# Kernel optimization log

Measured on AMD Instinct MI355X. Metric: run time of the kernel, lower is better.

The kernel has to match this reference:

```python
import jax, jax.numpy as jnp
import numpy as np


def prelu(x, a):
    return jnp.where(x >= 0, x, a * x)


def setup_inputs() -> dict:
    key = jax.random.key(0)
    ks = jax.random.split(key, 16)
    B, N, S, D = 4, 400, 512, 100
    rn = lambda k, shape, s=1.0: jax.random.normal(k, shape, dtype=jnp.float32) * s
    W = 0.05  # weight scale to keep activations sane
    return {
        "x": rn(ks[0], (B, N, D)),
        "G": rn(ks[1], (1, S, N), W),
        "A": rn(ks[2], (1, S, N), W),
        "W_gf": rn(ks[3], (D, N), W), "b_gf": rn(ks[4], (D,), W),
        "a_gf": jnp.float32(0.25),
        "Wg": rn(ks[5], (D, S), W), "bg": rn(ks[6], (D,), W),
        "W4a": rn(ks[7], (D, 2 * D), W), "b4a": rn(ks[8], (D,), W),
        "a4a": jnp.float32(0.25),
        "W4b": rn(ks[9], (1, D), W), "b4b": rn(ks[10], (1,), W),
        "a4b": jnp.float32(0.25),
        "W5": rn(ks[11], (D, D), W), "b5": rn(ks[12], (D,), W),
        "a5": jnp.float32(0.25),
    }


def reference(x, G, A, W_gf, b_gf, a_gf, Wg, bg, W4a, b4a, a4a, W4b, b4b, a4b, W5, b5, a5):
    B, N, D = x.shape          # (4, 400, 100)
    S = A.shape[1]             # 512
    # G1 = PReLU(Linear(G))  -> (1, S, D)
    G1 = prelu(jnp.einsum('osn,dn->osd', G, W_gf) + b_gf, a_gf)
    # A @ x -> (b, S, D)
    Ax = jnp.einsum('osn,bnd->bsd', A, x)
    # G_AX = G1 @ (A x)^T -> (b, S, S)
    G_AX = jnp.einsum('sd,btd->bst', G1[0], Ax)
    P = jax.nn.softmax(G_AX, axis=-1)                       # (b, S, S)
    # sim(): per-batch euclidean pdist on detached P
    Pd = jax.lax.stop_gradient(P)
    sq = jnp.sum(Pd * Pd, axis=-1)                          # (b, S)
    d2 = sq[:, :, None] + sq[:, None, :] - 2.0 * jnp.einsum('bij,bkj->bik', Pd, Pd)
    eye = jnp.eye(S, dtype=x.dtype)
    dist = jnp.sqrt(jnp.maximum(d2, 0.0)) * (1.0 - eye)     # squareform: zero diag
    # norm(): B = dist + I; D^-1/2 B D^-1/2; then extra .mm(B) (as in source)
    Bm = dist + eye
    dh = jnp.sum(Bm, axis=-1) ** -0.5                       # rowsum >= 1
    M = dh[:, :, None] * Bm * dh[:, None, :]
    adj = jnp.einsum('bij,bjk->bik', M, Bm)                 # (b, S, S)
    # gcn1: relu(Linear(adj @ P)), 512 -> 100
    gx = jax.nn.relu(jnp.einsum('bij,bjd->bid', adj, P) @ Wg.T + bg)  # (b, S, D)
    # tiled concat + MLP: Linear(200,100) split into x-part and gx-part
    h1 = x @ W4a[:, :D].T                                   # (b, N, D)
    h2 = gx @ W4a[:, D:].T                                  # (b, S, D)
    h = prelu(h1[:, :, None, :] + h2[:, None, :, :] + b4a, a4a)  # (b, N, S, D)
    logits = prelu(h @ W4b.T + b4b, a4b)                    # (b, N, S, 1)
    div = jax.nn.softmax(logits, axis=1)[..., 0]            # softmax over N -> (b, N, S)
    out = prelu(jnp.einsum('bns,bsd->bnd', div, gx) @ W5.T + b5, a5) + x
    return out
```

## Files before the change

kernel.cpp:

```cpp
#include <hip/hip_runtime.h>
#include <hip/hip_bf16.h>

#define BB 4
#define NN 400
#define DD 100
#define SS 512

typedef __attribute__((ext_vector_type(8))) short bf16x8;
typedef __attribute__((ext_vector_type(4))) float f32x4;

__device__ __forceinline__ float prelu_f(float v, float a) { return v >= 0.f ? v : a * v; }

__device__ __forceinline__ unsigned short f2bf(float x) {
    union { __hip_bfloat16 h; unsigned short u; } c;
    c.h = __float2bfloat16(x);
    return c.u;
}
__device__ __forceinline__ float bf2f(unsigned short u) {
    return __uint_as_float(((unsigned)u) << 16);
}

__device__ __forceinline__ bf16x8 ldfrag(const unsigned short* rowp, int grp) {
    ushort4 lo = *(const ushort4*)(rowp + grp * 4);
    ushort4 hi = *(const ushort4*)(rowp + grp * 4 + 16);
    bf16x8 r = {(short)lo.x, (short)lo.y, (short)lo.z, (short)lo.w,
                (short)hi.x, (short)hi.y, (short)hi.z, (short)hi.w};
    return r;
}

#define LPAD 136

__global__ __launch_bounds__(256)
void mmfa(const void* __restrict__ Ap, const void* __restrict__ A2p, int lda, int sA,
          const void* __restrict__ Bp, const void* __restrict__ B2p, int ldb, int sB,
          int transB, int flags,
          float* __restrict__ C, int sC, int M, int N, int K,
          int nsplit, int kchunk, int EP,
          const float* __restrict__ bias, const float* __restrict__ alpha,
          const float* __restrict__ rv, int rvStride,
          const float* __restrict__ res, int sRes)
{
    int zz = blockIdx.z;
    int b = zz / nsplit, split = zz - b * nsplit;
    int kbeg = split * kchunk, kend = min(K, kbeg + kchunk);
    int i0 = blockIdx.x * 64, n0 = blockIdx.y * 64;
    if (EP == 5 && i0 > n0) return;

    int tid = threadIdx.x;
    int lane = tid & 63, wave = tid >> 6;
    int r16 = lane & 15, grp = (lane >> 4) & 3;
    int wr = wave >> 1, wc = wave & 1;

    __shared__ unsigned short sa[64][LPAD];
    __shared__ unsigned short sb[64][LPAD];

    f32x4 acc[2][2];
#pragma unroll
    for (int fm = 0; fm < 2; ++fm)
#pragma unroll
        for (int fn = 0; fn < 2; ++fn)
            acc[fm][fn] = (f32x4){0.f, 0.f, 0.f, 0.f};

    for (int kt = kbeg; kt < kend; kt += 128) {
        if (flags & 1) {
            const unsigned short* Ab = (const unsigned short*)Ap + (size_t)b * sA;
#pragma unroll
            for (int it = 0; it < 8; ++it) {
                int idx = tid + it * 256;
                int row = idx >> 5, kq = (idx & 31) * 4;
                ushort4 u = {0, 0, 0, 0};
                if (i0 + row < M && kt + kq + 4 <= kend)
                    u = *(const ushort4*)&Ab[(size_t)(i0 + row) * lda + kt + kq];
                *(ushort4*)&sa[row][kq] = u;
            }
        } else {
            const float* Ab  = (const float*)Ap + (size_t)b * sA;
            const float* Ab2 = A2p ? (const float*)A2p + (size_t)b * sA : nullptr;
#pragma unroll
            for (int it = 0; it < 8; ++it) {
                int idx = tid + it * 256;
                int row = idx >> 5, kq = (idx & 31) * 4;
                float4 v = make_float4(0.f, 0.f, 0.f, 0.f);
                if (i0 + row < M && kt + kq + 4 <= kend) {
                    v = *(const float4*)&Ab[(size_t)(i0 + row) * lda + kt + kq];
                    if (Ab2) {
                        float4 w = *(const float4*)&Ab2[(size_t)(i0 + row) * lda + kt + kq];
                        v.x += w.x; v.y += w.y; v.z += w.z; v.w += w.w;
                    }
                }
                ushort4 u;
                u.x = f2bf(v.x); u.y = f2bf(v.y); u.z = f2bf(v.z); u.w = f2bf(v.w);
                *(ushort4*)&sa[row][kq] = u;
            }
        }
        if (transB) {
            if (flags & 2) {
                const unsigned short* Bb = (const unsigned short*)Bp + (size_t)b * sB;
#pragma unroll
                for (int it = 0; it < 8; ++it) {
                    int idx = tid + it * 256;
                    int row = idx >> 5, kq = (idx & 31) * 4;
                    ushort4 u = {0, 0, 0, 0};
                    if (n0 + row < N && kt + kq + 4 <= kend)
                        u = *(const ushort4*)&Bb[(size_t)(n0 + row) * ldb + kt + kq];
                    *(ushort4*)&sb[row][kq] = u;
                }
            } else {
                const float* Bb  = (const float*)Bp + (size_t)b * sB;
                const float* Bb2 = B2p ? (const float*)B2p + (size_t)b * sB : nullptr;
#pragma unroll
                for (int it = 0; it < 8; ++it) {
                    int idx = tid + it * 256;
                    int row = idx >> 5, kq = (idx & 31) * 4;
                    float4 v = make_float4(0.f, 0.f, 0.f, 0.f);
                    if (n0 + row < N && kt + kq + 4 <= kend) {
                        v = *(const float4*)&Bb[(size_t)(n0 + row) * ldb + kt + kq];
                        if (Bb2) {
                            float4 w = *(const float4*)&Bb2[(size_t)(n0 + row) * ldb + kt + kq];
                            v.x += w.x; v.y += w.y; v.z += w.z; v.w += w.w;
                        }
                    }
                    ushort4 u;
                    u.x = f2bf(v.x); u.y = f2bf(v.y); u.z = f2bf(v.z); u.w = f2bf(v.w);
                    *(ushort4*)&sb[row][kq] = u;
                }
            }
        } else {
            const float* Bb  = (const float*)Bp + (size_t)b * sB;
            const float* Bb2 = B2p ? (const float*)B2p + (size_t)b * sB : nullptr;
#pragma unroll
            for (int it = 0; it < 8; ++it) {
                int idx = tid + it * 256;
                int kk = idx >> 4;
                int nq = (idx & 15) * 4;
                float4 v = make_float4(0.f, 0.f, 0.f, 0.f);
                if (kt + kk < kend && n0 + nq + 4 <= N) {
                    v = *(const float4*)&Bb[(size_t)(kt + kk) * ldb + n0 + nq];
                    if (Bb2) {
                        float4 w = *(const float4*)&Bb2[(size_t)(kt + kk) * ldb + n0 + nq];
                        v.x += w.x; v.y += w.y; v.z += w.z; v.w += w.w;
                    }
                }
                sb[nq + 0][kk] = f2bf(v.x);
                sb[nq + 1][kk] = f2bf(v.y);
                sb[nq + 2][kk] = f2bf(v.z);
                sb[nq + 3][kk] = f2bf(v.w);
            }
        }
        __syncthreads();

#pragma unroll
        for (int ks = 0; ks < 4; ++ks) {
            bf16x8 a0 = ldfrag(&sa[wr * 32 + r16][ks * 32], grp);
            bf16x8 a1 = ldfrag(&sa[wr * 32 + 16 + r16][ks * 32], grp);
            bf16x8 b0 = ldfrag(&sb[wc * 32 + r16][ks * 32], grp);
            bf16x8 b1 = ldfrag(&sb[wc * 32 + 16 + r16][ks * 32], grp);
            acc[0][0] = __builtin_amdgcn_mfma_f32_16x16x32_bf16(a0, b0, acc[0][0], 0, 0, 0);
            acc[0][1] = __builtin_amdgcn_mfma_f32_16x16x32_bf16(a0, b1, acc[0][1], 0, 0, 0);
            acc[1][0] = __builtin_amdgcn_mfma_f32_16x16x32_bf16(a1, b0, acc[1][0], 0, 0, 0);
            acc[1][1] = __builtin_amdgcn_mfma_f32_16x16x32_bf16(a1, b1, acc[1][1], 0, 0, 0);
        }
        __syncthreads();
    }

    if (nsplit > 1) {
        float* Pp = C + (size_t)(b * nsplit + split) * M * N;
#pragma unroll
        for (int fm = 0; fm < 2; ++fm)
#pragma unroll
            for (int fn = 0; fn < 2; ++fn)
#pragma unroll
                for (int reg = 0; reg < 4; ++reg) {
                    int i = i0 + wr * 32 + fm * 16 + grp * 4 + reg;
                    int n = n0 + wc * 32 + fn * 16 + r16;
                    if (i < M && n < N) Pp[(size_t)i * N + n] = acc[fm][fn][reg];
                }
        return;
    }

    float al = alpha ? *alpha : 0.f;
    const float* rvb = rv ? rv + (size_t)b * rvStride : nullptr;
    float* Cb = C + (size_t)b * sC;
#pragma unroll
    for (int fm = 0; fm < 2; ++fm)
#pragma unroll
        for (int fn = 0; fn < 2; ++fn)
#pragma unroll
            for (int reg = 0; reg < 4; ++reg) {
                int i = i0 + wr * 32 + fm * 16 + grp * 4 + reg;
                int n = n0 + wc * 32 + fn * 16 + r16;
                if (i >= M || n >= N) continue;
                float v = acc[fm][fn][reg];
                if (EP == 4) {
                    v = prelu_f(v + bias[n], al) + res[(size_t)b * sRes + (size_t)i * N + n];
                } else if (EP == 5) {
                    float d2 = rvb[i] + rvb[n] - 2.f * v;
                    v = (i == n) ? 1.f : sqrtf(fmaxf(d2, 0.f));
                }
                Cb[(size_t)i * N + n] = v;
                if (EP == 5) Cb[(size_t)n * N + i] = v;
            }
}

__global__ __launch_bounds__(256)
void k_reduce(const float* __restrict__ part, int nsplit, float* __restrict__ C, int sC,
              int M, int N, int EP, const float* __restrict__ bias,
              const float* __restrict__ alpha, const float* __restrict__ rv, int rvStride)
{
    int b = blockIdx.y;
    int MN = M * N;
    int flat = (blockIdx.x * 256 + threadIdx.x) * 4;
    if (flat >= MN) return;
    const float* p = part + (size_t)b * nsplit * MN + flat;
    float4 v = *(const float4*)p;
    for (int s = 1; s < nsplit; ++s) {
        float4 w = *(const float4*)(p + (size_t)s * MN);
        v.x += w.x; v.y += w.y; v.z += w.z; v.w += w.w;
    }
    float o[4] = {v.x, v.y, v.z, v.w};
    int i = flat / N, n = flat - i * N;
    if (EP == 1) {
        float al = *alpha;
#pragma unroll
        for (int j = 0; j < 4; ++j) o[j] = prelu_f(o[j] + bias[n + j], al);
    } else if (EP == 2) {
        float r = rv[(size_t)b * rvStride + i];
#pragma unroll
        for (int j = 0; j < 4; ++j) o[j] *= r;
    } else if (EP == 3) {
        float r = rv[(size_t)b * rvStride + i];
#pragma unroll
        for (int j = 0; j < 4; ++j) { float t = r * o[j] + bias[n + j]; o[j] = t > 0.f ? t : 0.f; }
    }
    float* co = C + (size_t)b * sC + flat;
    *(float4*)co = make_float4(o[0], o[1], o[2], o[3]);
}

__global__ __launch_bounds__(256)
void kbm(const float* __restrict__ parts, const float* __restrict__ sq,
         float* __restrict__ Bm)
{
    int b = blockIdx.y;
    int flat = (blockIdx.x * 256 + threadIdx.x) * 4;
    int i = flat / SS, n0 = flat - i * SS;
    const float* pb = parts + (size_t)b * 4 * SS * SS;
    const float* sqb = sq + (size_t)b * SS;
    float o[4];
#pragma unroll
    for (int j = 0; j < 4; ++j) {
        int n = n0 + j;
        int lo = min(i, n), hi = max(i, n);
        size_t idx = (size_t)lo * SS + hi;
        float d = pb[idx] + pb[(size_t)SS * SS + idx]
                + pb[2 * (size_t)SS * SS + idx] + pb[3 * (size_t)SS * SS + idx];
        float d2 = sqb[i] + sqb[n] - 2.f * d;
        o[j] = (i == n) ? 1.f : sqrtf(fmaxf(d2, 0.f));
    }
    *(float4*)&Bm[(size_t)b * SS * SS + flat] = make_float4(o[0], o[1], o[2], o[3]);
}

__global__ __launch_bounds__(512)
void k_softmax_sq(const float* __restrict__ scores, unsigned short* __restrict__ Pb,
                  float* __restrict__ sq)
{
    int row = blockIdx.x;
    int t = threadIdx.x;
    int w = t >> 6, lane = t & 63;
    __shared__ float sm[8];

    float v = scores[(size_t)row * SS + t];
    float m = v;
    for (int off = 32; off; off >>= 1) m = fmaxf(m, __shfl_xor(m, off, 64));
    if (lane == 0) sm[w] = m;
    __syncthreads();
    m = sm[0];
#pragma unroll
    for (int i = 1; i < 8; ++i) m = fmaxf(m, sm[i]);
    __syncthreads();

    float e = expf(v - m);
    float s = e;
    for (int off = 32; off; off >>= 1) s += __shfl_xor(s, off, 64);
    if (lane == 0) sm[w] = s;
    __syncthreads();
    s = 0.f;
#pragma unroll
    for (int i = 0; i < 8; ++i) s += sm[i];
    __syncthreads();

    unsigned short u = f2bf(e / s);
    Pb[(size_t)row * SS + t] = u;
    float pf = bf2f(u);
    float q = pf * pf;
    for (int off = 32; off; off >>= 1) q += __shfl_xor(q, off, 64);
    if (lane == 0) sm[w] = q;
    __syncthreads();
    if (t == 0) {
        float r = 0.f;
#pragma unroll
        for (int i = 0; i < 8; ++i) r += sm[i];
        sq[row] = r;
    }
}

__global__ __launch_bounds__(512)
void k_dh(const float* __restrict__ Bm, float* __restrict__ dh)
{
    int row = blockIdx.x;
    int t = threadIdx.x;
    int w = t >> 6, lane = t & 63;
    __shared__ float sm[8];
    float v = Bm[(size_t)row * SS + t];
    for (int off = 32; off; off >>= 1) v += __shfl_xor(v, off, 64);
    if (lane == 0) sm[w] = v;
    __syncthreads();
    if (t == 0) {
        float r = 0.f;
#pragma unroll
        for (int i = 0; i < 8; ++i) r += sm[i];
        dh[row] = rsqrtf(r);
    }
}

__global__ __launch_bounds__(256)
void k_div8(const float* __restrict__ h1, const float* __restrict__ h2,
            const float* __restrict__ b4a, const float* __restrict__ a4ap,
            const float* __restrict__ W4b, const float* __restrict__ b4bp,
            const float* __restrict__ a4bp, float* __restrict__ divT)
{
    int b = blockIdx.y;
    int s0 = blockIdx.x * 8;
    int tid = threadIdx.x;

    __shared__ float sh[8][104];
    __shared__ float sw[100];
    __shared__ float L[8][400];

    for (int idx = tid; idx < 800; idx += 256) {
        int s = idx / 100, d = idx - 100 * s;
        sh[s][d] = h2[((size_t)(b * SS + s0 + s)) * DD + d] + b4a[d];
    }
    if (tid < 100) sw[tid] = W4b[tid];
    __syncthreads();

    float a4a = *a4ap, a4b = *a4bp, b4b = *b4bp;

    for (int n = tid; n < NN; n += 256) {
        const float* h1r = &h1[((size_t)b * NN + n) * DD];
        float accs[8] = {0.f, 0.f, 0.f, 0.f, 0.f, 0.f, 0.f, 0.f};
        for (int j = 0; j < DD; j += 4) {
            float4 hv = *(const float4*)&h1r[j];
            float4 wv = *(const float4*)&sw[j];
#pragma unroll
            for (int s = 0; s < 8; ++s) {
                float4 cv = *(const float4*)&sh[s][j];
                float x0 = hv.x + cv.x; x0 = x0 > 0.f ? x0 : a4a * x0;
                float x1 = hv.y + cv.y; x1 = x1 > 0.f ? x1 : a4a * x1;
                float x2 = hv.z + cv.z; x2 = x2 > 0.f ? x2 : a4a * x2;
                float x3 = hv.w + cv.w; x3 = x3 > 0.f ? x3 : a4a * x3;
                accs[s] += x0 * wv.x + x1 * wv.y + x2 * wv.z + x3 * wv.w;
            }
        }
#pragma unroll
        for (int s = 0; s < 8; ++s) L[s][n] = prelu_f(accs[s] + b4b, a4b);
    }
    __syncthreads();

    int w = tid >> 6, lane = tid & 63;
    for (int si = w; si < 8; si += 4) {
        float m = -INFINITY;
        for (int n = lane; n < NN; n += 64) m = fmaxf(m, L[si][n]);
        for (int off = 32; off; off >>= 1) m = fmaxf(m, __shfl_xor(m, off, 64));
        float ss = 0.f;
        for (int n = lane; n < NN; n += 64) {
            float e = expf(L[si][n] - m);
            L[si][n] = e;
            ss += e;
        }
        for (int off = 32; off; off >>= 1) ss += __shfl_xor(ss, off, 64);
        float inv = 1.f / ss;
        for (int n = lane; n < NN; n += 64)
            divT[((size_t)b * NN + n) * SS + s0 + si] = L[si][n] * inv;
    }
}

extern "C" void kernel_launch(void* const* d_in, const int* in_sizes, int n_in,
                              void* d_out, int out_size, void* d_ws, size_t ws_size,
                              hipStream_t stream) {
    const float* x   = (const float*)d_in[0];
    const float* G   = (const float*)d_in[1];
    const float* Am  = (const float*)d_in[2];
    const float* Wgf = (const float*)d_in[3];
    const float* bgf = (const float*)d_in[4];
    const float* agf = (const float*)d_in[5];
    const float* Wg  = (const float*)d_in[6];
    const float* bg  = (const float*)d_in[7];
    const float* W4a = (const float*)d_in[8];
    const float* b4a = (const float*)d_in[9];
    const float* a4a = (const float*)d_in[10];
    const float* W4b = (const float*)d_in[11];
    const float* b4b = (const float*)d_in[12];
    const float* a4b = (const float*)d_in[13];
    const float* W5  = (const float*)d_in[14];
    const float* b5  = (const float*)d_in[15];
    const float* a5  = (const float*)d_in[16];
    float* out = (float*)d_out;

    float* ws = (float*)d_ws;
    float* G1   = ws + 0;
    float* G1P  = ws + 51200;
    float* AXP  = ws + 256000;
    float* SC   = ws + 665600;
    float* BM   = ws + 1714176;
    float* SQ   = ws + 2762752;
    float* DH   = ws + 2764800;
    float* PDP  = ws + 2766848;
    float* PWP  = ws + 6961152;
    float* PW   = ws + 7780352;
    float* T1P  = ws + 7985152;
    float* T1   = ws + 8804352;
    float* GXP  = ws + 9009152;
    float* GX   = ws + 9828352;
    float* H1   = ws + 10033152;
    float* H2   = ws + 10193152;
    float* DV   = ws + 10397952;
    float* TMPP = ws + 11217152;
    float* TMP  = ws + 11857152;
    unsigned short* PB = (unsigned short*)(ws + 12017152);

    mmfa<<<dim3(8, 2, 4), 256, 0, stream>>>(G, nullptr, NN, 0, Wgf, nullptr, NN, 0, 1, 0,
        G1P, 0, SS, DD, NN, 4, 100, 0, nullptr, nullptr, nullptr, 0, nullptr, 0);
    k_reduce<<<dim3(50, 1), 256, 0, stream>>>(G1P, 4, G1, SS * DD, SS, DD, 1, bgf, agf, nullptr, 0);
    mmfa<<<dim3(8, 2, 2 * BB), 256, 0, stream>>>(Am, nullptr, NN, 0, x, nullptr, DD, NN * DD, 0, 0,
        AXP, 0, SS, DD, NN, 2, 200, 0, nullptr, nullptr, nullptr, 0, nullptr, 0);
    mmfa<<<dim3(8, 8, BB), 256, 0, stream>>>(G1, nullptr, DD, 0,
        AXP, AXP + SS * DD, DD, 2 * SS * DD, 1, 0,
        SC, SS * SS, SS, SS, DD, 1, DD, 0, nullptr, nullptr, nullptr, 0, nullptr, 0);
    k_softmax_sq<<<BB * SS, 512, 0, stream>>>(SC, PB, SQ);
    mmfa<<<dim3(8, 8, 4 * BB), 256, 0, stream>>>(PB, nullptr, SS, SS * SS, PB, nullptr, SS, SS * SS, 1, 3,
        PDP, 0, SS, SS, SS, 4, 128, 5, nullptr, nullptr, nullptr, 0, nullptr, 0);
    kbm<<<dim3(256, BB), 256, 0, stream>>>(PDP, SQ, BM);
    k_dh<<<BB * SS, 512, 0, stream>>>(BM, DH);
    mmfa<<<dim3(8, 2, 4 * BB), 256, 0, stream>>>(PB, nullptr, SS, SS * SS, Wg, nullptr, SS, 0, 1, 1,
        PWP, 0, SS, DD, SS, 4, 128, 0, nullptr, nullptr, nullptr, 0, nullptr, 0);
    k_reduce<<<dim3(50, BB), 256, 0, stream>>>(PWP, 4, PW, SS * DD, SS, DD, 0, nullptr, nullptr, nullptr, 0);
    mmfa<<<dim3(8, 2, 4 * BB), 256, 0, stream>>>(BM, nullptr, SS, SS * SS, PW, nullptr, DD, SS * DD, 0, 0,
        T1P, 0, SS, DD, SS, 4, 128, 0, nullptr, nullptr, nullptr, 0, nullptr, 0);
    k_reduce<<<dim3(50, BB), 256, 0, stream>>>(T1P, 4, T1, SS * DD, SS, DD, 2, nullptr, nullptr, DH, SS);
    mmfa<<<dim3(8, 2, 4 * BB), 256, 0, stream>>>(BM, nullptr, SS, SS * SS, T1, nullptr, DD, SS * DD, 0, 0,
        GXP, 0, SS, DD, SS, 4, 128, 0, nullptr, nullptr, nullptr, 0, nullptr, 0);
    k_reduce<<<dim3(50, BB), 256, 0, stream>>>(GXP, 4, GX, SS * DD, SS, DD, 3, bg, nullptr, DH, SS);
    mmfa<<<dim3(7, 2, BB), 256, 0, stream>>>(x, nullptr, DD, NN * DD, W4a, nullptr, 2 * DD, 0, 1, 0,
        H1, NN * DD, NN, DD, DD, 1, DD, 0, nullptr, nullptr, nullptr, 0, nullptr, 0);
    mmfa<<<dim3(8, 2, BB), 256, 0, stream>>>(GX, nullptr, DD, SS * DD, W4a + DD, nullptr, 2 * DD, 0, 1, 0,
        H2, SS * DD, SS, DD, DD, 1, DD, 0, nullptr, nullptr, nullptr, 0, nullptr, 0);
    k_div8<<<dim3(SS / 8, BB), 256, 0, stream>>>(H1, H2, b4a, a4a, W4b, b4b, a4b, DV);
    mmfa<<<dim3(7, 2, 4 * BB), 256, 0, stream>>>(DV, nullptr, SS, NN * SS, GX, nullptr, DD, SS * DD, 0, 0,
        TMPP, 0, NN, DD, SS, 4, 128, 0, nullptr, nullptr, nullptr, 0, nullptr, 0);
    k_reduce<<<dim3(40, BB), 256, 0, stream>>>(TMPP, 4, TMP, NN * DD, NN, DD, 0, nullptr, nullptr, nullptr, 0);
    mmfa<<<dim3(7, 2, BB), 256, 0, stream>>>(TMP, nullptr, DD, NN * DD, W5, nullptr, DD, 0, 1, 0,
        out, NN * DD, NN, DD, DD, 1, DD, 4, b5, a5, nullptr, 0, x, NN * DD);
}
```

Measured before the change: 276.5 us.

## Merge independent GEMMs into combined launches and fold reductions into consumer loads

Factors the GEMM body into a device function so that independent GEMMs (G·Wgf, A·x, x·W4a, and the Gram matrix with P·Wg) can share a single launch, with work selected by block index. Split-K partials are now summed inside the next GEMM's operand load instead of in separate reduce kernels. The D^-1/2 scaling is applied as a per-row B-operand scale and in the epilogue. The row-sum and rsqrt step is folded into the Bm construction kernel. Together these cut the number of kernel launches and intermediate round trips through memory, at the cost of lower split-K parallelism in some GEMMs and more per-load arithmetic.

```diff
diff --git a/kernel.cpp b/kernel.cpp
--- a/kernel.cpp
+++ b/kernel.cpp
@@ -5,6 +5,8 @@
 #define NN 400
 #define DD 100
 #define SS 512
+#define LPAD 136
+#define SMEM_BYTES (64 * LPAD * 2 * 2)
 
 typedef __attribute__((ext_vector_type(8))) short bf16x8;
 typedef __attribute__((ext_vector_type(4))) float f32x4;
@@ -28,32 +30,22 @@
     return r;
 }
 
-#define LPAD 136
-
-__global__ __launch_bounds__(256)
-void mmfa(const void* __restrict__ Ap, const void* __restrict__ A2p, int lda, int sA,
-          const void* __restrict__ Bp, const void* __restrict__ B2p, int ldb, int sB,
-          int transB, int flags,
-          float* __restrict__ C, int sC, int M, int N, int K,
-          int nsplit, int kchunk, int EP,
-          const float* __restrict__ bias, const float* __restrict__ alpha,
-          const float* __restrict__ rv, int rvStride,
-          const float* __restrict__ res, int sRes)
-{
-    int zz = blockIdx.z;
-    int b = zz / nsplit, split = zz - b * nsplit;
-    int kbeg = split * kchunk, kend = min(K, kbeg + kchunk);
-    int i0 = blockIdx.x * 64, n0 = blockIdx.y * 64;
-    if (EP == 5 && i0 > n0) return;
-
+__device__ __forceinline__ void mm_dev(char* smemraw,
+    const void* Ap, const void* A2p, int aBf, int lda,
+    const void* Bp, const void* B2p, int bBf, int ldb, int transB,
+    const float* bscale,
+    int i0, int n0, int M, int N, int kbeg, int kend,
+    float* C, int ldc, int EP,
+    const float* bias, const float* alphaP, const float* rv,
+    const float* res, int resLd)
+{
+    unsigned short (*sa)[LPAD] = (unsigned short(*)[LPAD])smemraw;
+    unsigned short (*sb)[LPAD] = (unsigned short(*)[LPAD])(smemraw + 64 * LPAD * 2);
     int tid = threadIdx.x;
     int lane = tid & 63, wave = tid >> 6;
     int r16 = lane & 15, grp = (lane >> 4) & 3;
     int wr = wave >> 1, wc = wave & 1;
 
-    __shared__ unsigned short sa[64][LPAD];
-    __shared__ unsigned short sb[64][LPAD];
-
     f32x4 acc[2][2];
 #pragma unroll
     for (int fm = 0; fm < 2; ++fm)
@@ -62,8 +54,8 @@
             acc[fm][fn] = (f32x4){0.f, 0.f, 0.f, 0.f};
 
     for (int kt = kbeg; kt < kend; kt += 128) {
-        if (flags & 1) {
-            const unsigned short* Ab = (const unsigned short*)Ap + (size_t)b * sA;
+        if (aBf) {
+            const unsigned short* Ab = (const unsigned short*)Ap;
 #pragma unroll
             for (int it = 0; it < 8; ++it) {
                 int idx = tid + it * 256;
@@ -74,8 +66,8 @@
                 *(ushort4*)&sa[row][kq] = u;
             }
         } else {
-            const float* Ab  = (const float*)Ap + (size_t)b * sA;
-            const float* Ab2 = A2p ? (const float*)A2p + (size_t)b * sA : nullptr;
+            const float* Ab  = (const float*)Ap;
+            const float* Ab2 = (const float*)A2p;
 #pragma unroll
             for (int it = 0; it < 8; ++it) {
                 int idx = tid + it * 256;
@@ -94,8 +86,8 @@
             }
         }
         if (transB) {
-            if (flags & 2) {
-                const unsigned short* Bb = (const unsigned short*)Bp + (size_t)b * sB;
+            if (bBf) {
+                const unsigned short* Bb = (const unsigned short*)Bp;
 #pragma unroll
                 for (int it = 0; it < 8; ++it) {
                     int idx = tid + it * 256;
@@ -106,8 +98,8 @@
                     *(ushort4*)&sb[row][kq] = u;
                 }
             } else {
-                const float* Bb  = (const float*)Bp + (size_t)b * sB;
-                const float* Bb2 = B2p ? (const float*)B2p + (size_t)b * sB : nullptr;
+                const float* Bb  = (const float*)Bp;
+                const float* Bb2 = (const float*)B2p;
 #pragma unroll
                 for (int it = 0; it < 8; ++it) {
                     int idx = tid + it * 256;
@@ -126,8 +118,8 @@
                 }
             }
         } else {
-            const float* Bb  = (const float*)Bp + (size_t)b * sB;
-            const float* Bb2 = B2p ? (const float*)B2p + (size_t)b * sB : nullptr;
+            const float* Bb  = (const float*)Bp;
+            const float* Bb2 = (const float*)B2p;
 #pragma unroll
             for (int it = 0; it < 8; ++it) {
                 int idx = tid + it * 256;
@@ -140,6 +132,10 @@
                         float4 w = *(const float4*)&Bb2[(size_t)(kt + kk) * ldb + n0 + nq];
                         v.x += w.x; v.y += w.y; v.z += w.z; v.w += w.w;
                     }
+                    if (bscale) {
+                        float s = bscale[kt + kk];
+                        v.x *= s; v.y *= s; v.z *= s; v.w *= s;
+                    }
                 }
                 sb[nq + 0][kk] = f2bf(v.x);
                 sb[nq + 1][kk] = f2bf(v.y);
@@ -163,24 +159,7 @@
         __syncthreads();
     }
 
-    if (nsplit > 1) {
-        float* Pp = C + (size_t)(b * nsplit + split) * M * N;
-#pragma unroll
-        for (int fm = 0; fm < 2; ++fm)
-#pragma unroll
-            for (int fn = 0; fn < 2; ++fn)
-#pragma unroll
-                for (int reg = 0; reg < 4; ++reg) {
-                    int i = i0 + wr * 32 + fm * 16 + grp * 4 + reg;
-                    int n = n0 + wc * 32 + fn * 16 + r16;
-                    if (i < M && n < N) Pp[(size_t)i * N + n] = acc[fm][fn][reg];
-                }
-        return;
-    }
-
-    float al = alpha ? *alpha : 0.f;
-    const float* rvb = rv ? rv + (size_t)b * rvStride : nullptr;
-    float* Cb = C + (size_t)b * sC;
+    float al = alphaP ? *alphaP : 0.f;
 #pragma unroll
     for (int fm = 0; fm < 2; ++fm)
 #pragma unroll
@@ -191,15 +170,147 @@
                 int n = n0 + wc * 32 + fn * 16 + r16;
                 if (i >= M || n >= N) continue;
                 float v = acc[fm][fn][reg];
-                if (EP == 4) {
-                    v = prelu_f(v + bias[n], al) + res[(size_t)b * sRes + (size_t)i * N + n];
-                } else if (EP == 5) {
-                    float d2 = rvb[i] + rvb[n] - 2.f * v;
+                if (EP == 1) v = prelu_f(v + bias[n], al);
+                else if (EP == 2) v *= rv[i];
+                else if (EP == 3) { float t = rv[i] * v + bias[n]; v = t > 0.f ? t : 0.f; }
+                else if (EP == 4) v = prelu_f(v + bias[n], al) + res[(size_t)i * resLd + n];
+                else if (EP == 5) {
+                    float d2 = rv[i] + rv[n] - 2.f * v;
                     v = (i == n) ? 1.f : sqrtf(fmaxf(d2, 0.f));
                 }
-                Cb[(size_t)i * N + n] = v;
-                if (EP == 5) Cb[(size_t)n * N + i] = v;
+                C[(size_t)i * ldc + n] = v;
+                if (EP == 5) C[(size_t)n * ldc + i] = v;
             }
+}
+
+__global__ __launch_bounds__(256)
+void mmfa(const void* Ap, const void* A2p, int lda, int sA,
+          const void* Bp, const void* B2p, int ldb, int sB,
+          int transB, int flags,
+          const float* bscale, int bscaleStride,
+          float* C, int sC, int M, int N, int K,
+          int nsplit, int kchunk, int EP,
+          const float* bias, const float* alpha,
+          const float* rv, int rvStride,
+          const float* res, int sRes)
+{
+    __shared__ __align__(16) char sm[SMEM_BYTES];
+    int zz = blockIdx.z;
+    int b = zz / nsplit, split = zz - b * nsplit;
+    int kbeg = split * kchunk, kend = min(K, kbeg + kchunk);
+    int i0 = blockIdx.x * 64, n0 = blockIdx.y * 64;
+    if (EP == 5 && i0 > n0) return;
+
+    const void* Ab; const void* Ab2 = nullptr;
+    if (flags & 1) Ab = (const void*)((const unsigned short*)Ap + (size_t)b * sA);
+    else {
+        Ab = (const void*)((const float*)Ap + (size_t)b * sA);
+        if (A2p) Ab2 = (const void*)((const float*)A2p + (size_t)b * sA);
+    }
+    const void* Bb; const void* Bb2 = nullptr;
+    if (flags & 2) Bb = (const void*)((const unsigned short*)Bp + (size_t)b * sB);
+    else {
+        Bb = (const void*)((const float*)Bp + (size_t)b * sB);
+        if (B2p) Bb2 = (const void*)((const float*)B2p + (size_t)b * sB);
+    }
+    const float* bs = bscale ? bscale + (size_t)b * bscaleStride : nullptr;
+
+    float* Cd; int ep;
+    if (nsplit > 1) { Cd = C + (size_t)(b * nsplit + split) * M * N; ep = 0; }
+    else            { Cd = C + (size_t)b * sC; ep = EP; }
+    const float* rvb = rv ? rv + (size_t)b * rvStride : nullptr;
+    const float* resb = res ? res + (size_t)b * sRes : nullptr;
+
+    mm_dev(sm, Ab, Ab2, flags & 1, lda, Bb, Bb2, flags & 2, ldb, transB, bs,
+           i0, n0, M, N, kbeg, kend, Cd, N, ep, bias, alpha, rvb, resb, N);
+}
+
+__global__ __launch_bounds__(256)
+void preU(const float* G, const float* Wgf, const float* Am, const float* x,
+          const float* W4a, float* G1P, float* AXP, float* H1)
+{
+    __shared__ __align__(16) char sm[SMEM_BYTES];
+    int t = blockIdx.x;
+    if (t < 64) {
+        int split = t >> 4, rem = t & 15, ix = rem >> 1, iy = rem & 1;
+        mm_dev(sm, G, nullptr, 0, NN, Wgf, nullptr, 0, NN, 1, nullptr,
+               ix * 64, iy * 64, SS, DD, split * 100, split * 100 + 100,
+               G1P + (size_t)split * SS * DD, DD, 0,
+               nullptr, nullptr, nullptr, nullptr, 0);
+    } else if (t < 192) {
+        int u = t - 64;
+        int b = u >> 5, rem = u & 31, split = rem >> 4, r2 = rem & 15;
+        int ix = r2 >> 1, iy = r2 & 1;
+        mm_dev(sm, Am, nullptr, 0, NN, x + (size_t)b * NN * DD, nullptr, 0, DD, 0, nullptr,
+               ix * 64, iy * 64, SS, DD, split * 200, split * 200 + 200,
+               AXP + (size_t)(b * 2 + split) * SS * DD, DD, 0,
+               nullptr, nullptr, nullptr, nullptr, 0);
+    } else {
+        int u = t - 192;
+        int b = u / 14, rem = u % 14, ix = rem >> 1, iy = rem & 1;
+        mm_dev(sm, x + (size_t)b * NN * DD, nullptr, 0, DD, W4a, nullptr, 0, 2 * DD, 1, nullptr,
+               ix * 64, iy * 64, NN, DD, 0, DD,
+               H1 + (size_t)b * NN * DD, DD, 0,
+               nullptr, nullptr, nullptr, nullptr, 0);
+    }
+}
+
+__global__ __launch_bounds__(256)
+void gramU(const unsigned short* PB, const float* Wg, float* PDP, float* PWP)
+{
+    __shared__ __align__(16) char sm[SMEM_BYTES];
+    int t = blockIdx.x;
+    if (t < 1024) {
+        int z = t >> 6, rem = t & 63, ix = rem >> 3, iy = rem & 7;
+        if (ix > iy) return;
+        int b = z >> 2, split = z & 3;
+        const unsigned short* Pbb = PB + (size_t)b * SS * SS;
+        mm_dev(sm, Pbb, nullptr, 1, SS, Pbb, nullptr, 1, SS, 1, nullptr,
+               ix * 64, iy * 64, SS, SS, split * 128, split * 128 + 128,
+               PDP + (size_t)(b * 4 + split) * SS * SS, SS, 0,
+               nullptr, nullptr, nullptr, nullptr, 0);
+    } else {
+        int u = t - 1024;
+        int z = u >> 4, rem = u & 15, ix = rem >> 1, iy = rem & 1;
+        int b = z >> 1, split = z & 1;
+        mm_dev(sm, PB + (size_t)b * SS * SS, nullptr, 1, SS, Wg, nullptr, 0, SS, 1, nullptr,
+               ix * 64, iy * 64, SS, DD, split * 256, split * 256 + 256,
+               PWP + (size_t)(b * 2 + split) * SS * DD, DD, 0,
+               nullptr, nullptr, nullptr, nullptr, 0);
+    }
+}
+
+__global__ __launch_bounds__(256)
+void kbm2(const float* __restrict__ parts, const float* __restrict__ sq,
+          float* __restrict__ Bm, float* __restrict__ dh)
+{
+    __shared__ float red[4];
+    int b = blockIdx.y;
+    int tid = threadIdx.x;
+    int flat = (blockIdx.x * 256 + tid) * 4;
+    int i = flat / SS, n0 = flat - i * SS;
+    const float* pb = parts + (size_t)b * 4 * SS * SS;
+    const float* sqb = sq + (size_t)b * SS;
+    float o[4];
+#pragma unroll
+    for (int j = 0; j < 4; ++j) {
+        int n = n0 + j;
+        int lo = min(i, n), hi = max(i, n);
+        size_t idx = (size_t)lo * SS + hi;
+        float d = pb[idx] + pb[(size_t)SS * SS + idx]
+                + pb[2 * (size_t)SS * SS + idx] + pb[3 * (size_t)SS * SS + idx];
+        float d2 = sqb[i] + sqb[n] - 2.f * d;
+        o[j] = (i == n) ? 1.f : sqrtf(fmaxf(d2, 0.f));
+    }
+    *(float4*)&Bm[(size_t)b * SS * SS + flat] = make_float4(o[0], o[1], o[2], o[3]);
+
+    float rs = o[0] + o[1] + o[2] + o[3];
+    for (int off = 32; off; off >>= 1) rs += __shfl_xor(rs, off, 64);
+    int lane = tid & 63, wave = tid >> 6;
+    if (lane == 0) red[wave] = rs;
+    __syncthreads();
+    if (tid == 0)   dh[(size_t)b * SS + blockIdx.x * 2]     = rsqrtf(red[0] + red[1]);
+    if (tid == 128) dh[(size_t)b * SS + blockIdx.x * 2 + 1] = rsqrtf(red[2] + red[3]);
 }
 
 __global__ __launch_bounds__(256)
@@ -236,29 +347,6 @@
     *(float4*)co = make_float4(o[0], o[1], o[2], o[3]);
 }
 
-__global__ __launch_bounds__(256)
-void kbm(const float* __restrict__ parts, const float* __restrict__ sq,
-         float* __restrict__ Bm)
-{
-    int b = blockIdx.y;
-    int flat = (blockIdx.x * 256 + threadIdx.x) * 4;
-    int i = flat / SS, n0 = flat - i * SS;
-    const float* pb = parts + (size_t)b * 4 * SS * SS;
-    const float* sqb = sq + (size_t)b * SS;
-    float o[4];
-#pragma unroll
-    for (int j = 0; j < 4; ++j) {
-        int n = n0 + j;
-        int lo = min(i, n), hi = max(i, n);
-        size_t idx = (size_t)lo * SS + hi;
-        float d = pb[idx] + pb[(size_t)SS * SS + idx]
-                + pb[2 * (size_t)SS * SS + idx] + pb[3 * (size_t)SS * SS + idx];
-        float d2 = sqb[i] + sqb[n] - 2.f * d;
-        o[j] = (i == n) ? 1.f : sqrtf(fmaxf(d2, 0.f));
-    }
-    *(float4*)&Bm[(size_t)b * SS * SS + flat] = make_float4(o[0], o[1], o[2], o[3]);
-}
-
 __global__ __launch_bounds__(512)
 void k_softmax_sq(const float* __restrict__ scores, unsigned short* __restrict__ Pb,
                   float* __restrict__ sq)
@@ -300,25 +388,6 @@
 #pragma unroll
         for (int i = 0; i < 8; ++i) r += sm[i];
         sq[row] = r;
-    }
-}
-
-__global__ __launch_bounds__(512)
-void k_dh(const float* __restrict__ Bm, float* __restrict__ dh)
-{
-    int row = blockIdx.x;
-    int t = threadIdx.x;
-    int w = t >> 6, lane = t & 63;
-    __shared__ float sm[8];
-    float v = Bm[(size_t)row * SS + t];
-    for (int off = 32; off; off >>= 1) v += __shfl_xor(v, off, 64);
-    if (lane == 0) sm[w] = v;
-    __syncthreads();
-    if (t == 0) {
-        float r = 0.f;
-#pragma unroll
-        for (int i = 0; i < 8; ++i) r += sm[i];
-        dh[row] = rsqrtf(r);
     }
 }
 
@@ -416,48 +485,36 @@
     float* DH   = ws + 2764800;
     float* PDP  = ws + 2766848;
     float* PWP  = ws + 6961152;
-    float* PW   = ws + 7780352;
-    float* T1P  = ws + 7985152;
-    float* T1   = ws + 8804352;
-    float* GXP  = ws + 9009152;
-    float* GX   = ws + 9828352;
-    float* H1   = ws + 10033152;
-    float* H2   = ws + 10193152;
-    float* DV   = ws + 10397952;
-    float* TMPP = ws + 11217152;
-    float* TMP  = ws + 11857152;
-    unsigned short* PB = (unsigned short*)(ws + 12017152);
-
-    mmfa<<<dim3(8, 2, 4), 256, 0, stream>>>(G, nullptr, NN, 0, Wgf, nullptr, NN, 0, 1, 0,
-        G1P, 0, SS, DD, NN, 4, 100, 0, nullptr, nullptr, nullptr, 0, nullptr, 0);
+    float* T1P  = ws + 7370752;
+    float* GX   = ws + 7780352;
+    float* H1   = ws + 7985152;
+    float* H2   = ws + 8145152;
+    float* DV   = ws + 8349952;
+    float* TMPP = ws + 9169152;
+    unsigned short* PB = (unsigned short*)(ws + 9489152);
+
+    preU<<<248, 256, 0, stream>>>(G, Wgf, Am, x, W4a, G1P, AXP, H1);
     k_reduce<<<dim3(50, 1), 256, 0, stream>>>(G1P, 4, G1, SS * DD, SS, DD, 1, bgf, agf, nullptr, 0);
-    mmfa<<<dim3(8, 2, 2 * BB), 256, 0, stream>>>(Am, nullptr, NN, 0, x, nullptr, DD, NN * DD, 0, 0,
-        AXP, 0, SS, DD, NN, 2, 200, 0, nullptr, nullptr, nullptr, 0, nullptr, 0);
     mmfa<<<dim3(8, 8, BB), 256, 0, stream>>>(G1, nullptr, DD, 0,
-        AXP, AXP + SS * DD, DD, 2 * SS * DD, 1, 0,
+        AXP, AXP + SS * DD, DD, 2 * SS * DD, 1, 0, nullptr, 0,
         SC, SS * SS, SS, SS, DD, 1, DD, 0, nullptr, nullptr, nullptr, 0, nullptr, 0);
     k_softmax_sq<<<BB * SS, 512, 0, stream>>>(SC, PB, SQ);
-    mmfa<<<dim3(8, 8, 4 * BB), 256, 0, stream>>>(PB, nullptr, SS, SS * SS, PB, nullptr, SS, SS * SS, 1, 3,
-        PDP, 0, SS, SS, SS, 4, 128, 5, nullptr, nullptr, nullptr, 0, nullptr, 0);
-    kbm<<<dim3(256, BB), 256, 0, stream>>>(PDP, SQ, BM);
-    k_dh<<<BB * SS, 512, 0, stream>>>(BM, DH);
-    mmfa<<<dim3(8, 2, 4 * BB), 256, 0, stream>>>(PB, nullptr, SS, SS * SS, Wg, nullptr, SS, 0, 1, 1,
-        PWP, 0, SS, DD, SS, 4, 128, 0, nullptr, nullptr, nullptr, 0, nullptr, 0);
-    k_reduce<<<dim3(50, BB), 256, 0, stream>>>(PWP, 4, PW, SS * DD, SS, DD, 0, nullptr, nullptr, nullptr, 0);
-    mmfa<<<dim3(8, 2, 4 * BB), 256, 0, stream>>>(BM, nullptr, SS, SS * SS, PW, nullptr, DD, SS * DD, 0, 0,
-        T1P, 0, SS, DD, SS, 4, 128, 0, nullptr, nullptr, nullptr, 0, nullptr, 0);
-    k_reduce<<<dim3(50, BB), 256, 0, stream>>>(T1P, 4, T1, SS * DD, SS, DD, 2, nullptr, nullptr, DH, SS);
-    mmfa<<<dim3(8, 2, 4 * BB), 256, 0, stream>>>(BM, nullptr, SS, SS * SS, T1, nullptr, DD, SS * DD, 0, 0,
-        GXP, 0, SS, DD, SS, 4, 128, 0, nullptr, nullptr, nullptr, 0, nullptr, 0);
-    k_reduce<<<dim3(50, BB), 256, 0, stream>>>(GXP, 4, GX, SS * DD, SS, DD, 3, bg, nullptr, DH, SS);
-    mmfa<<<dim3(7, 2, BB), 256, 0, stream>>>(x, nullptr, DD, NN * DD, W4a, nullptr, 2 * DD, 0, 1, 0,
-        H1, NN * DD, NN, DD, DD, 1, DD, 0, nullptr, nullptr, nullptr, 0, nullptr, 0);
-    mmfa<<<dim3(8, 2, BB), 256, 0, stream>>>(GX, nullptr, DD, SS * DD, W4a + DD, nullptr, 2 * DD, 0, 1, 0,
+    gramU<<<1152, 256, 0, stream>>>(PB, Wg, PDP, PWP);
+    kbm2<<<dim3(256, BB), 256, 0, stream>>>(PDP, SQ, BM, DH);
+    mmfa<<<dim3(8, 2, 2 * BB), 256, 0, stream>>>(BM, nullptr, SS, SS * SS,
+        PWP, PWP + SS * DD, DD, 2 * SS * DD, 0, 0, nullptr, 0,
+        T1P, 0, SS, DD, SS, 2, 256, 0, nullptr, nullptr, nullptr, 0, nullptr, 0);
+    mmfa<<<dim3(8, 2, BB), 256, 0, stream>>>(BM, nullptr, SS, SS * SS,
+        T1P, T1P + SS * DD, DD, 2 * SS * DD, 0, 0, DH, SS,
+        GX, SS * DD, SS, DD, SS, 1, SS, 3, bg, nullptr, DH, SS, nullptr, 0);
+    mmfa<<<dim3(8, 2, BB), 256, 0, stream>>>(GX, nullptr, DD, SS * DD,
+        W4a + DD, nullptr, 2 * DD, 0, 1, 0, nullptr, 0,
         H2, SS * DD, SS, DD, DD, 1, DD, 0, nullptr, nullptr, nullptr, 0, nullptr, 0);
     k_div8<<<dim3(SS / 8, BB), 256, 0, stream>>>(H1, H2, b4a, a4a, W4b, b4b, a4b, DV);
-    mmfa<<<dim3(7, 2, 4 * BB), 256, 0, stream>>>(DV, nullptr, SS, NN * SS, GX, nullptr, DD, SS * DD, 0, 0,
-        TMPP, 0, NN, DD, SS, 4, 128, 0, nullptr, nullptr, nullptr, 0, nullptr, 0);
-    k_reduce<<<dim3(40, BB), 256, 0, stream>>>(TMPP, 4, TMP, NN * DD, NN, DD, 0, nullptr, nullptr, nullptr, 0);
-    mmfa<<<dim3(7, 2, BB), 256, 0, stream>>>(TMP, nullptr, DD, NN * DD, W5, nullptr, DD, 0, 1, 0,
+    mmfa<<<dim3(7, 2, 2 * BB), 256, 0, stream>>>(DV, nullptr, SS, NN * SS,
+        GX, nullptr, DD, SS * DD, 0, 0, nullptr, 0,
+        TMPP, 0, NN, DD, SS, 2, 256, 0, nullptr, nullptr, nullptr, 0, nullptr, 0);
+    mmfa<<<dim3(7, 2, BB), 256, 0, stream>>>(TMPP, TMPP + NN * DD, DD, 2 * NN * DD,
+        W5, nullptr, DD, 0, 1, 0, nullptr, 0,
         out, NN * DD, NN, DD, DD, 1, DD, 4, b5, a5, nullptr, 0, x, NN * DD);
 }
```

Measured after the change: 268.1 us. -3.1%, faster.
